# Kernel optimization log

Measured on AMD Instinct MI355X. Metric: run time of the kernel, lower is better.

## Reference

```python
import jax, jax.numpy as jnp
import numpy as np

B, D, H = 32, 512, 1024


def setup_inputs() -> dict:
    key = jax.random.key(0)
    ks = jax.random.split(key, 9)
    x = jax.random.normal(ks[0], (B, D), dtype=jnp.float32)
    h0 = 0.1 * jax.random.normal(ks[1], (B, H), dtype=jnp.float32)
    c0 = 0.1 * jax.random.normal(ks[2], (B, H), dtype=jnp.float32)
    # Hebbian trace lives in [-1, 1] (clipped each step)
    Hebb0 = jax.random.uniform(ks[3], (B, H, H), dtype=jnp.float32, minval=-0.5, maxval=0.5)
    weight_h = jax.random.normal(ks[4], (H, 4 * H), dtype=jnp.float32) / np.sqrt(H)
    weight_x = jax.random.normal(ks[5], (D, 4 * H), dtype=jnp.float32) / np.sqrt(D)
    # bias init: zeros, forget-gate slice set to 1 (T_max=None path)
    bias = jnp.zeros((4 * H,), dtype=jnp.float32).at[:H].set(1.0)
    # alpha init is constant 0.01; add tiny noise for non-degenerate testing
    alpha = 0.01 + 0.001 * jax.random.normal(ks[6], (H, H), dtype=jnp.float32)
    eta = jnp.array([0.01], dtype=jnp.float32)
    return {"x": x, "h0": h0, "c0": c0, "Hebb0": Hebb0,
            "weight_h": weight_h, "weight_x": weight_x, "bias": bias,
            "alpha": alpha, "eta": eta}


def reference(x, h0, c0, Hebb0, weight_h, weight_x, bias, alpha, eta):
    Hs = h0.shape[1]
    # gates = h0 @ (weight_h + cat[0,0,0, alpha*Hebb]) + x @ weight_x + bias
    # The plastic term only affects the last (cell-gate) chunk; compute it
    # without materializing the (B,H,4H) dynamic weight tensor.
    gates = h0 @ weight_h + x @ weight_x + bias[None, :]
    plastic = jnp.einsum('bi,ih,bih->bh', h0, alpha, Hebb0)  # (B, H)
    f_g, i_g, o_g, g_g = jnp.split(gates, 4, axis=1)
    g_g = g_g + plastic  # cell gate gets the fast-weight contribution
    tanh_g = jnp.tanh(g_g)
    c1 = jax.nn.sigmoid(f_g) * c0 + jax.nn.sigmoid(i_g) * tanh_g
    h1 = jax.nn.sigmoid(o_g) * jnp.tanh(c1)
    # Hebbian outer-product update with clip (neuromodulation=None path)
    Hebb1 = jnp.clip(Hebb0 + eta[0] * jnp.einsum('bh,bi->bhi', h0, tanh_g), -1.0, 1.0)
    return h1, c1, Hebb1
```

## Files before the change

kernel.cpp:

```cpp
#include <hip/hip_runtime.h>
#include <math.h>

#define B 32
#define D 512
#define H 1024
#define G4 4096
#define PCH 64
#define GCH 48

typedef float f4v __attribute__((ext_vector_type(4)));

__global__ __launch_bounds__(256) void k_plastic(
    const float* __restrict__ h0, const float* __restrict__ alpha,
    const float* __restrict__ hebb, float* __restrict__ pp) {
  int blk = blockIdx.x;
  int b = blk >> 6;
  int c = blk & (PCH - 1);
  int h4 = threadIdx.x * 4;
  int i0 = c * (H / PCH);
  const float* hb = hebb + (size_t)b * H * H;
  float4 acc = make_float4(0.f, 0.f, 0.f, 0.f);
#pragma unroll
  for (int half = 0; half < 2; ++half) {
    int ib = i0 + half * 8;
    float4 ev[8], av[8];
    float hv[8];
#pragma unroll
    for (int u = 0; u < 8; ++u)
      ev[u] = *(const float4*)(hb + (size_t)(ib + u) * H + h4);
#pragma unroll
    for (int u = 0; u < 8; ++u)
      av[u] = *(const float4*)(alpha + (size_t)(ib + u) * H + h4);
#pragma unroll
    for (int u = 0; u < 8; ++u) hv[u] = h0[b * H + ib + u];
#pragma unroll
    for (int u = 0; u < 8; ++u) {
      acc.x += hv[u] * av[u].x * ev[u].x;
      acc.y += hv[u] * av[u].y * ev[u].y;
      acc.z += hv[u] * av[u].z * ev[u].z;
      acc.w += hv[u] * av[u].w * ev[u].w;
    }
  }
  *(float4*)(pp + ((size_t)c * B + b) * H + h4) = acc;
}

__global__ __launch_bounds__(256) void k_gates(
    const float* __restrict__ h0, const float* __restrict__ x,
    const float* __restrict__ wh, const float* __restrict__ wx,
    float* __restrict__ gp) {
  int j = blockIdx.x * 256 + threadIdx.x;
  int c = blockIdx.y;
  const float* Wp;
  const float* in;
  int i0, ld;
  if (c < 32) { Wp = wh; in = h0; i0 = c * 32; ld = H; }
  else        { Wp = wx; in = x;  i0 = (c - 32) * 32; ld = D; }
  float acc[B];
#pragma unroll
  for (int b = 0; b < B; ++b) acc[b] = 0.f;
#pragma unroll
  for (int uo = 0; uo < 4; ++uo) {
    float w[8];
#pragma unroll
    for (int u = 0; u < 8; ++u)
      w[u] = Wp[(size_t)(i0 + uo * 8 + u) * G4 + j];
#pragma unroll
    for (int u = 0; u < 8; ++u) {
      int i = i0 + uo * 8 + u;
#pragma unroll
      for (int b = 0; b < B; ++b) acc[b] += in[b * ld + i] * w[u];
    }
  }
#pragma unroll
  for (int b = 0; b < B; ++b) gp[((size_t)c * B + b) * G4 + j] = acc[b];
}

__global__ __launch_bounds__(64) void k_combine(
    const float* __restrict__ gp, const float* __restrict__ pp,
    const float* __restrict__ bias, const float* __restrict__ c0,
    float* __restrict__ out, float* __restrict__ tg_out) {
  int t = blockIdx.x * 64 + threadIdx.x;
  int b = t >> 10;
  int h = t & (H - 1);
  float sf = bias[h], si = bias[H + h], so = bias[2 * H + h], sg = bias[3 * H + h];
#pragma unroll
  for (int c8 = 0; c8 < GCH / 8; ++c8) {
    float vf[8], vi[8], vo[8], vg[8];
#pragma unroll
    for (int u = 0; u < 8; ++u) {
      const float* g = gp + ((size_t)(c8 * 8 + u) * B + b) * G4;
      vf[u] = g[h];
      vi[u] = g[H + h];
      vo[u] = g[2 * H + h];
      vg[u] = g[3 * H + h];
    }
#pragma unroll
    for (int u = 0; u < 8; ++u) { sf += vf[u]; si += vi[u]; so += vo[u]; sg += vg[u]; }
  }
#pragma unroll
  for (int c16 = 0; c16 < PCH / 16; ++c16) {
    float vp[16];
#pragma unroll
    for (int u = 0; u < 16; ++u)
      vp[u] = pp[((size_t)(c16 * 16 + u) * B + b) * H + h];
#pragma unroll
    for (int u = 0; u < 16; ++u) sg += vp[u];
  }
  float fg = 1.f / (1.f + expf(-sf));
  float ig = 1.f / (1.f + expf(-si));
  float og = 1.f / (1.f + expf(-so));
  float tgv = tanhf(sg);
  float c1 = fg * c0[t] + ig * tgv;
  float h1 = og * tanhf(c1);
  out[t] = h1;
  out[B * H + t] = c1;
  tg_out[t] = tgv;
}

__global__ __launch_bounds__(256) void k_hebb(
    const float* __restrict__ hebb, const float* __restrict__ h0,
    const float* __restrict__ tg, const float* __restrict__ eta,
    float* __restrict__ out) {
  int blk = blockIdx.x;
  int b = blk >> 7;
  int hg = blk & 127;
  int t4 = threadIdx.x * 4;
  float4 tv = *(const float4*)(tg + b * H + t4);
  float e = eta[0];
  size_t base = ((size_t)b * H + (size_t)hg * 8) * H + t4;
  const float* src = hebb + base;
  float* dst = out + base;
  float4 v[8];
  float s[8];
#pragma unroll
  for (int r = 0; r < 8; ++r)
    v[r] = *(const float4*)(src + (size_t)r * H);
#pragma unroll
  for (int r = 0; r < 8; ++r)
    s[r] = e * h0[b * H + hg * 8 + r];
#pragma unroll
  for (int r = 0; r < 8; ++r) {
    f4v rr;
    rr.x = fminf(fmaxf(v[r].x + s[r] * tv.x, -1.f), 1.f);
    rr.y = fminf(fmaxf(v[r].y + s[r] * tv.y, -1.f), 1.f);
    rr.z = fminf(fmaxf(v[r].z + s[r] * tv.z, -1.f), 1.f);
    rr.w = fminf(fmaxf(v[r].w + s[r] * tv.w, -1.f), 1.f);
    __builtin_nontemporal_store(rr, (f4v*)(dst + (size_t)r * H));
  }
}

extern "C" void kernel_launch(void* const* d_in, const int* in_sizes, int n_in,
                              void* d_out, int out_size, void* d_ws, size_t ws_size,
                              hipStream_t stream) {
  const float* x     = (const float*)d_in[0];
  const float* h0    = (const float*)d_in[1];
  const float* c0    = (const float*)d_in[2];
  const float* hebb  = (const float*)d_in[3];
  const float* wh    = (const float*)d_in[4];
  const float* wx    = (const float*)d_in[5];
  const float* bias  = (const float*)d_in[6];
  const float* alpha = (const float*)d_in[7];
  const float* eta   = (const float*)d_in[8];
  float* out = (float*)d_out;
  float* ws  = (float*)d_ws;

  float* pp = ws;
  float* gp = pp + (size_t)PCH * B * H;
  float* tg = gp + (size_t)GCH * B * G4;

  k_plastic<<<B * PCH, 256, 0, stream>>>(h0, alpha, hebb, pp);
  k_gates<<<dim3(16, GCH), 256, 0, stream>>>(h0, x, wh, wx, gp);
  k_combine<<<(B * H) / 64, 64, 0, stream>>>(gp, pp, bias, c0, out, tg);
  k_hebb<<<B * 128, 256, 0, stream>>>(hebb, h0, tg, eta, out + 2 * B * H);
}
```

Measured before the change: 316.3 us.

## Merge plastic and gate GEMV kernels into one launch with fewer partial chunks

```diff
diff --git a/kernel.cpp b/kernel.cpp
--- a/kernel.cpp
+++ b/kernel.cpp
@@ -5,81 +5,83 @@
 #define D 512
 #define H 1024
 #define G4 4096
-#define PCH 64
-#define GCH 48
+#define PCH 32
+#define GCH 24
+#define NGATE (16 * GCH)
 
 typedef float f4v __attribute__((ext_vector_type(4)));
 
-__global__ __launch_bounds__(256) void k_plastic(
-    const float* __restrict__ h0, const float* __restrict__ alpha,
-    const float* __restrict__ hebb, float* __restrict__ pp) {
+__global__ __launch_bounds__(256) void k_pg(
+    const float* __restrict__ h0, const float* __restrict__ x,
+    const float* __restrict__ wh, const float* __restrict__ wx,
+    const float* __restrict__ alpha, const float* __restrict__ hebb,
+    float* __restrict__ gp, float* __restrict__ pp) {
   int blk = blockIdx.x;
-  int b = blk >> 6;
-  int c = blk & (PCH - 1);
-  int h4 = threadIdx.x * 4;
-  int i0 = c * (H / PCH);
-  const float* hb = hebb + (size_t)b * H * H;
-  float4 acc = make_float4(0.f, 0.f, 0.f, 0.f);
+  int tid = threadIdx.x;
+  if (blk < NGATE) {
+    int c = blk % GCH;
+    int j = (blk / GCH) * 256 + tid;
+    const float* Wp;
+    const float* in;
+    int i0, ld;
+    if (c < 16) { Wp = wh; in = h0; i0 = c * 64; ld = H; }
+    else        { Wp = wx; in = x;  i0 = (c - 16) * 64; ld = D; }
+    float acc[B];
 #pragma unroll
-  for (int half = 0; half < 2; ++half) {
-    int ib = i0 + half * 8;
-    float4 ev[8], av[8];
-    float hv[8];
+    for (int b = 0; b < B; ++b) acc[b] = 0.f;
 #pragma unroll
-    for (int u = 0; u < 8; ++u)
-      ev[u] = *(const float4*)(hb + (size_t)(ib + u) * H + h4);
+    for (int uo = 0; uo < 8; ++uo) {
+      float w[8];
 #pragma unroll
-    for (int u = 0; u < 8; ++u)
-      av[u] = *(const float4*)(alpha + (size_t)(ib + u) * H + h4);
+      for (int u = 0; u < 8; ++u)
+        w[u] = Wp[(size_t)(i0 + uo * 8 + u) * G4 + j];
 #pragma unroll
-    for (int u = 0; u < 8; ++u) hv[u] = h0[b * H + ib + u];
+      for (int u = 0; u < 8; ++u) {
+        int i = i0 + uo * 8 + u;
 #pragma unroll
-    for (int u = 0; u < 8; ++u) {
-      acc.x += hv[u] * av[u].x * ev[u].x;
-      acc.y += hv[u] * av[u].y * ev[u].y;
-      acc.z += hv[u] * av[u].z * ev[u].z;
-      acc.w += hv[u] * av[u].w * ev[u].w;
+        for (int b = 0; b < B; ++b) acc[b] += in[b * ld + i] * w[u];
+      }
     }
+#pragma unroll
+    for (int b = 0; b < B; ++b) gp[((size_t)c * B + b) * G4 + j] = acc[b];
+  } else {
+    int p = blk - NGATE;
+    int b = p & (B - 1);
+    int c = p >> 5;
+    int h4 = tid * 4;
+    int i0 = c * (H / PCH);
+    const float* hb = hebb + (size_t)b * H * H;
+    float4 acc = make_float4(0.f, 0.f, 0.f, 0.f);
+#pragma unroll
+    for (int quad = 0; quad < 4; ++quad) {
+      int ib = i0 + quad * 8;
+      float4 ev[8], av[8];
+      float hv[8];
+#pragma unroll
+      for (int u = 0; u < 8; ++u)
+        ev[u] = *(const float4*)(hb + (size_t)(ib + u) * H + h4);
+#pragma unroll
+      for (int u = 0; u < 8; ++u)
+        av[u] = *(const float4*)(alpha + (size_t)(ib + u) * H + h4);
+#pragma unroll
+      for (int u = 0; u < 8; ++u) hv[u] = h0[b * H + ib + u];
+#pragma unroll
+      for (int u = 0; u < 8; ++u) {
+        acc.x += hv[u] * av[u].x * ev[u].x;
+        acc.y += hv[u] * av[u].y * ev[u].y;
+        acc.z += hv[u] * av[u].z * ev[u].z;
+        acc.w += hv[u] * av[u].w * ev[u].w;
+      }
+    }
+    *(float4*)(pp + ((size_t)c * B + b) * H + h4) = acc;
   }
-  *(float4*)(pp + ((size_t)c * B + b) * H + h4) = acc;
 }
 
-__global__ __launch_bounds__(256) void k_gates(
-    const float* __restrict__ h0, const float* __restrict__ x,
-    const float* __restrict__ wh, const float* __restrict__ wx,
-    float* __restrict__ gp) {
-  int j = blockIdx.x * 256 + threadIdx.x;
-  int c = blockIdx.y;
-  const float* Wp;
-  const float* in;
-  int i0, ld;
-  if (c < 32) { Wp = wh; in = h0; i0 = c * 32; ld = H; }
-  else        { Wp = wx; in = x;  i0 = (c - 32) * 32; ld = D; }
-  float acc[B];
-#pragma unroll
-  for (int b = 0; b < B; ++b) acc[b] = 0.f;
-#pragma unroll
-  for (int uo = 0; uo < 4; ++uo) {
-    float w[8];
-#pragma unroll
-    for (int u = 0; u < 8; ++u)
-      w[u] = Wp[(size_t)(i0 + uo * 8 + u) * G4 + j];
-#pragma unroll
-    for (int u = 0; u < 8; ++u) {
-      int i = i0 + uo * 8 + u;
-#pragma unroll
-      for (int b = 0; b < B; ++b) acc[b] += in[b * ld + i] * w[u];
-    }
-  }
-#pragma unroll
-  for (int b = 0; b < B; ++b) gp[((size_t)c * B + b) * G4 + j] = acc[b];
-}
-
-__global__ __launch_bounds__(64) void k_combine(
+__global__ __launch_bounds__(256) void k_combine(
     const float* __restrict__ gp, const float* __restrict__ pp,
     const float* __restrict__ bias, const float* __restrict__ c0,
     float* __restrict__ out, float* __restrict__ tg_out) {
-  int t = blockIdx.x * 64 + threadIdx.x;
+  int t = blockIdx.x * 256 + threadIdx.x;
   int b = t >> 10;
   int h = t & (H - 1);
   float sf = bias[h], si = bias[H + h], so = bias[2 * H + h], sg = bias[3 * H + h];
@@ -89,22 +91,19 @@
 #pragma unroll
     for (int u = 0; u < 8; ++u) {
       const float* g = gp + ((size_t)(c8 * 8 + u) * B + b) * G4;
-      vf[u] = g[h];
-      vi[u] = g[H + h];
-      vo[u] = g[2 * H + h];
-      vg[u] = g[3 * H + h];
+      vf[u] = g[h]; vi[u] = g[H + h]; vo[u] = g[2 * H + h]; vg[u] = g[3 * H + h];
     }
 #pragma unroll
     for (int u = 0; u < 8; ++u) { sf += vf[u]; si += vi[u]; so += vo[u]; sg += vg[u]; }
   }
 #pragma unroll
-  for (int c16 = 0; c16 < PCH / 16; ++c16) {
-    float vp[16];
+  for (int c8 = 0; c8 < PCH / 8; ++c8) {
+    float vp[8];
 #pragma unroll
-    for (int u = 0; u < 16; ++u)
-      vp[u] = pp[((size_t)(c16 * 16 + u) * B + b) * H + h];
+    for (int u = 0; u < 8; ++u)
+      vp[u] = pp[((size_t)(c8 * 8 + u) * B + b) * H + h];
 #pragma unroll
-    for (int u = 0; u < 16; ++u) sg += vp[u];
+    for (int u = 0; u < 8; ++u) sg += vp[u];
   }
   float fg = 1.f / (1.f + expf(-sf));
   float ig = 1.f / (1.f + expf(-si));
@@ -168,8 +167,7 @@
   float* gp = pp + (size_t)PCH * B * H;
   float* tg = gp + (size_t)GCH * B * G4;
 
-  k_plastic<<<B * PCH, 256, 0, stream>>>(h0, alpha, hebb, pp);
-  k_gates<<<dim3(16, GCH), 256, 0, stream>>>(h0, x, wh, wx, gp);
-  k_combine<<<(B * H) / 64, 64, 0, stream>>>(gp, pp, bias, c0, out, tg);
+  k_pg<<<NGATE + B * PCH, 256, 0, stream>>>(h0, x, wh, wx, alpha, hebb, gp, pp);
+  k_combine<<<(B * H) / 256, 256, 0, stream>>>(gp, pp, bias, c0, out, tg);
   k_hebb<<<B * 128, 256, 0, stream>>>(hebb, h0, tg, eta, out + 2 * B * H);
 }
```

Measured after the change: 297.5 us. 1.06x faster.
